# Performance work log

Measured on AMD Instinct MI355X. Metric: run time of the kernel, lower is better.

The kernel has to match this reference:

```python
import jax, jax.numpy as jnp
import numpy as np

B, T, F, H = 64, 512, 128, 512
NUM_LAYERS = 3


def _lstm_layer(x_tbf, W_ih, W_hh, b_ih, b_hh):
    # x_tbf: [T, B, in], W_ih: [4H, in], W_hh: [4H, H]
    # PyTorch gate order: i, f, g, o
    Hd = W_hh.shape[1]
    Bd = x_tbf.shape[1]
    # precompute input projections for all timesteps (one big GEMM)
    x_proj = jnp.einsum('tbf,gf->tbg', x_tbf, W_ih) + b_ih  # [T, B, 4H]

    def step(carry, xp_t):
        h, c = carry
        gates = xp_t + h @ W_hh.T + b_hh  # [B, 4H]
        i, f, g, o = jnp.split(gates, 4, axis=-1)
        i = jax.nn.sigmoid(i)
        f = jax.nn.sigmoid(f)
        g = jnp.tanh(g)
        o = jax.nn.sigmoid(o)
        c = f * c + i * g
        h = o * jnp.tanh(c)
        return (h, c), h

    h0 = jnp.zeros((Bd, Hd), x_tbf.dtype)
    c0 = jnp.zeros((Bd, Hd), x_tbf.dtype)
    _, hs = jax.lax.scan(step, (h0, c0), x_proj)
    return hs  # [T, B, H]


def setup_inputs() -> dict:
    key = jax.random.key(0)
    ks = jax.random.split(key, 20)
    s = 1.0 / np.sqrt(H)
    inp = {"input_tensor": jax.random.normal(ks[0], (B, T, F), jnp.float32)}
    in_dims = [F, H, H]
    ki = 1
    for l in range(NUM_LAYERS):
        inp[f"W_ih{l}"] = jax.random.uniform(ks[ki], (4 * H, in_dims[l]), jnp.float32, -s, s); ki += 1
        inp[f"W_hh{l}"] = jax.random.uniform(ks[ki], (4 * H, H), jnp.float32, -s, s); ki += 1
        inp[f"b_ih{l}"] = jax.random.uniform(ks[ki], (4 * H,), jnp.float32, -s, s); ki += 1
        inp[f"b_hh{l}"] = jax.random.uniform(ks[ki], (4 * H,), jnp.float32, -s, s); ki += 1
    s1 = 1.0 / np.sqrt(H)
    inp["fc_W1"] = jax.random.uniform(ks[13], (64, H), jnp.float32, -s1, s1)
    inp["fc_b1"] = jax.random.uniform(ks[14], (64,), jnp.float32, -s1, s1)
    s2 = 1.0 / np.sqrt(64)
    inp["fc_W2"] = jax.random.uniform(ks[15], (1, 64), jnp.float32, -s2, s2)
    inp["fc_b2"] = jax.random.uniform(ks[16], (1,), jnp.float32, -s2, s2)
    return inp


def reference(input_tensor, W_ih0, W_hh0, b_ih0, b_hh0,
              W_ih1, W_hh1, b_ih1, b_hh1,
              W_ih2, W_hh2, b_ih2, b_hh2,
              fc_W1, fc_b1, fc_W2, fc_b2):
    x = jnp.transpose(input_tensor, (1, 0, 2))  # [T, B, F]
    x = _lstm_layer(x, W_ih0, W_hh0, b_ih0, b_hh0)
    x = _lstm_layer(x, W_ih1, W_hh1, b_ih1, b_hh1)  # eval mode: no dropout
    x = _lstm_layer(x, W_ih2, W_hh2, b_ih2, b_hh2)
    last = x[-1]  # [B, H]
    h1 = jax.nn.relu(last @ fc_W1.T + fc_b1)
    out = jax.nn.relu(h1 @ fc_W2.T + fc_b2)  # [B, 1]
    return out
```

## Files before the change

### kernel.cpp

```cpp
#include <hip/hip_runtime.h>
#include <hip/hip_fp16.h>
#include <math.h>

#define B_ 64
#define T_ 512
#define F_ 128
#define H_ 512
#define NBLK 96
#define SPIN_MAX (1 << 23)

typedef _Float16 f16x8 __attribute__((ext_vector_type(8)));
typedef float f32x4 __attribute__((ext_vector_type(4)));
typedef int   i32x4 __attribute__((ext_vector_type(4)));

__device__ __forceinline__ unsigned short f2h(float f) {
    return __half_as_ushort(__float2half(f));
}
__device__ __forceinline__ float h2f(unsigned short u) {
    return __half2float(__ushort_as_half(u));
}

__global__ void transpose_x(const float* __restrict__ in, unsigned* __restrict__ xs) {
    const int t = blockIdx.x;
    for (int idx = threadIdx.x; idx < B_ * F_ / 4; idx += blockDim.x) {
        const int kp2 = idx >> 6;
        const int bb = idx & 63;
        const float* src = in + (size_t)bb * T_ * F_ + (size_t)t * F_ + 4 * kp2;
        const unsigned h0 = f2h(src[0]), h1 = f2h(src[1]);
        const unsigned h2 = f2h(src[2]), h3 = f2h(src[3]);
        const unsigned dw0 = h0 | (h1 << 16);
        const unsigned dw1 = h2 | (h3 << 16);
        *(unsigned long long*)(xs + (size_t)t * 4096 + (size_t)kp2 * 128 + bb * 2) =
            ((unsigned long long)dw1 << 32) | dw0;
    }
}

__device__ __forceinline__ float sigmoid_(float x) { return 1.0f / (1.0f + expf(-x)); }

__device__ __forceinline__ unsigned long long loadc_u64(const unsigned* p) {
    return __hip_atomic_load((const unsigned long long*)p, __ATOMIC_RELAXED,
                             __HIP_MEMORY_SCOPE_AGENT);
}
__device__ __forceinline__ unsigned loadc_u32(const unsigned* p) {
    return __hip_atomic_load(p, __ATOMIC_RELAXED, __HIP_MEMORY_SCOPE_AGENT);
}
__device__ __forceinline__ void storec_u64(unsigned* p, unsigned long long v) {
    __hip_atomic_store((unsigned long long*)p, v, __ATOMIC_RELAXED,
                       __HIP_MEMORY_SCOPE_AGENT);
}
__device__ __forceinline__ void storec_f(float* p, float v) {
    __hip_atomic_store(p, v, __ATOMIC_RELAXED, __HIP_MEMORY_SCOPE_AGENT);
}
__device__ __forceinline__ float loadc_f(const float* p) {
    return __hip_atomic_load(p, __ATOMIC_RELAXED, __HIP_MEMORY_SCOPE_AGENT);
}

__device__ __forceinline__ void gbar(int* __restrict__ slots, int* __restrict__ go,
                                     int bid, int tid, int e) {
    asm volatile("s_waitcnt vmcnt(0) lgkmcnt(0)" ::: "memory");
    __syncthreads();
    if (tid == 0)
        __hip_atomic_store(&slots[bid * 16], e, __ATOMIC_RELAXED,
                           __HIP_MEMORY_SCOPE_AGENT);
    if (bid == 0) {
        for (int s2 = tid; s2 < NBLK; s2 += 256) {
            int guard = 0;
            while (__hip_atomic_load(&slots[s2 * 16], __ATOMIC_RELAXED,
                                     __HIP_MEMORY_SCOPE_AGENT) < e &&
                   ++guard < SPIN_MAX)
                __builtin_amdgcn_s_sleep(1);
        }
        __syncthreads();
        if (tid == 0)
            __hip_atomic_store(go, e, __ATOMIC_RELAXED, __HIP_MEMORY_SCOPE_AGENT);
    } else if (tid == 0) {
        int guard = 0;
        while (__hip_atomic_load(go, __ATOMIC_RELAXED,
                                 __HIP_MEMORY_SCOPE_AGENT) < e &&
               ++guard < SPIN_MAX)
            __builtin_amdgcn_s_sleep(1);
    }
    __syncthreads();
}

template <int NKX, bool XCOH>
__device__ __forceinline__ void step_mfma(const unsigned* __restrict__ xs_l,
                                          const unsigned* __restrict__ hs_l,
                                          const unsigned short* wfrag,
                                          const int lane, f32x4 (&acc)[4]) {
    constexpr int NK = NKX + 16;
    unsigned long long v[8][2];

    auto load2 = [&](unsigned long long* d, int i) {
        const unsigned* p = (i < NKX) ? (xs_l + (size_t)i * 1024)
                                      : (hs_l + (size_t)(i - NKX) * 1024);
        if ((i < NKX) ? XCOH : true) {
            d[0] = loadc_u64(p);
            d[1] = loadc_u64(p + 128);
        } else {
            d[0] = *(const unsigned long long*)p;
            d[1] = *(const unsigned long long*)(p + 128);
        }
    };

#pragma unroll
    for (int p = 0; p < 8; ++p) load2(v[p], p);

#pragma unroll
    for (int i = 0; i < NK; ++i) {
        union Frag { i32x4 i4; f16x8 s; } Bf, A0, A1, A2, A3;
        const unsigned long long* d = v[i % 8];
        Bf.i4[0] = (int)(unsigned)d[0];
        Bf.i4[1] = (int)(unsigned)(d[0] >> 32);
        Bf.i4[2] = (int)(unsigned)d[1];
        Bf.i4[3] = (int)(unsigned)(d[1] >> 32);
        if (i + 8 < NK) load2(v[i % 8], i + 8);
        A0.i4 = *(const i32x4*)&wfrag[i * 2048 + lane * 8];
        A1.i4 = *(const i32x4*)&wfrag[i * 2048 + 512 + lane * 8];
        A2.i4 = *(const i32x4*)&wfrag[i * 2048 + 1024 + lane * 8];
        A3.i4 = *(const i32x4*)&wfrag[i * 2048 + 1536 + lane * 8];
        acc[0] = __builtin_amdgcn_mfma_f32_16x16x32_f16(A0.s, Bf.s, acc[0], 0, 0, 0);
        acc[1] = __builtin_amdgcn_mfma_f32_16x16x32_f16(A1.s, Bf.s, acc[1], 0, 0, 0);
        acc[2] = __builtin_amdgcn_mfma_f32_16x16x32_f16(A2.s, Bf.s, acc[2], 0, 0, 0);
        acc[3] = __builtin_amdgcn_mfma_f32_16x16x32_f16(A3.s, Bf.s, acc[3], 0, 0, 0);
    }
}

__global__ void __launch_bounds__(256, 1) lstm_scan(
    const unsigned* __restrict__ xs, unsigned* __restrict__ hb,
    float* __restrict__ h1s, float* __restrict__ out,
    int* __restrict__ bar_slots, int* __restrict__ bar_go,
    const float* __restrict__ Wih0, const float* __restrict__ Whh0,
    const float* __restrict__ bih0, const float* __restrict__ bhh0,
    const float* __restrict__ Wih1, const float* __restrict__ Whh1,
    const float* __restrict__ bih1, const float* __restrict__ bhh1,
    const float* __restrict__ Wih2, const float* __restrict__ Whh2,
    const float* __restrict__ bih2, const float* __restrict__ bhh2,
    const float* __restrict__ fcW1, const float* __restrict__ fcb1,
    const float* __restrict__ fcW2, const float* __restrict__ fcb2) {
    __shared__ unsigned short wfrag[32 * 2048];
    __shared__ float redsc[4 * 64];

    const float* WihA[3] = {Wih0, Wih1, Wih2};
    const float* WhhA[3] = {Whh0, Whh1, Whh2};
    const float* bihA[3] = {bih0, bih1, bih2};
    const float* bhhA[3] = {bhh0, bhh1, bhh2};

    const int tid   = threadIdx.x;
    const int bid   = blockIdx.x;
    const int layer = bid >> 5;
    const int cb    = bid & 31;
    const int c0    = cb * 16;
    const int lane  = tid & 63;
    const int w     = __builtin_amdgcn_readfirstlane(tid >> 6);
    const int KX    = (layer == 0) ? F_ : H_;
    const int NK    = KX / 32 + 16;

    const float* wih = WihA[layer];
    const float* whh = WhhA[layer];

    for (int idx = tid; idx < NK * 2048; idx += 256) {
        const int i = idx >> 11, rem = idx & 2047;
        const int rg = rem >> 9, r2 = rem & 511;
        const int l = r2 >> 3, j = r2 & 7;
        const int m = l & 15;
        const int grow = (m & 3) * 512 + c0 + rg * 4 + (m >> 2);
        const int k = i * 32 + (l >> 4) * 8 + j;
        const float f = (k < KX) ? wih[(size_t)grow * KX + k]
                                 : whh[(size_t)grow * 512 + (k - KX)];
        wfrag[i * 2048 + rg * 512 + l * 8 + j] = f2h(f);
    }
    __syncthreads();

    const int fb    = w * 16 + (lane & 15);
    const int q     = lane >> 4;
    float bias[4][4];
#pragma unroll
    for (int rg = 0; rg < 4; ++rg)
#pragma unroll
        for (int g = 0; g < 4; ++g)
            bias[rg][g] = bihA[layer][g * 512 + c0 + rg * 4 + q] +
                          bhhA[layer][g * 512 + c0 + rg * 4 + q];

    unsigned* hb_l = hb + (size_t)layer * 32768;
    const unsigned* hb_in = hb + (size_t)(layer - 1) * 32768;
    int hstore[4];
#pragma unroll
    for (int rg = 0; rg < 4; ++rg)
        hstore[rg] = (cb * 4 + rg) * 128 + fb * 2;

    float c_reg[4] = {0.0f, 0.0f, 0.0f, 0.0f};
    const int laneoff = q * 256 + fb * 2;

    for (int s = 0; s < T_ + 2; ++s) {
        const int t = s - layer;
        if (t >= 0 && t < T_) {
            const int p_out  = t & 1;
            const int p_prev = (t + 1) & 1;
            const unsigned* xs_l =
                ((layer == 0) ? (xs + (size_t)t * 4096)
                              : (hb_in + (size_t)p_out * 16384)) + laneoff;
            const unsigned* hs_l = hb_l + (size_t)p_prev * 16384 + laneoff;

            f32x4 acc[4] = {{0.f,0.f,0.f,0.f},{0.f,0.f,0.f,0.f},
                            {0.f,0.f,0.f,0.f},{0.f,0.f,0.f,0.f}};
            if (layer == 0) step_mfma<4, false>(xs_l, hs_l, wfrag, lane, acc);
            else            step_mfma<16, true>(xs_l, hs_l, wfrag, lane, acc);

#pragma unroll
            for (int rg = 0; rg < 4; ++rg) {
                float a[4];
#pragma unroll
                for (int g = 0; g < 4; ++g)
                    a[g] = bias[rg][g] + acc[rg][g];

                const float ig = sigmoid_(a[0]);
                const float fg = sigmoid_(a[1]);
                const float gg = tanhf(a[2]);
                const float og = sigmoid_(a[3]);
                c_reg[rg] = fg * c_reg[rg] + ig * gg;
                const float hv = og * tanhf(c_reg[rg]);

                const unsigned P0 = (unsigned)f2h(hv);
                const unsigned P1 = (unsigned)__shfl_xor((int)P0, 16, 64) & 0xFFFFu;
                const unsigned D  = P0 | (P1 << 16);
                const unsigned D2 = (unsigned)__shfl_xor((int)D, 32, 64);
                if (q == 0) {
                    storec_u64(&hb_l[(size_t)p_out * 16384 + hstore[rg]],
                               ((unsigned long long)D2 << 32) | D);
                }
            }
        }
        gbar(bar_slots, bar_go, bid, tid, s + 1);
    }

    const unsigned* h2u = hb + (size_t)2 * 32768 + 16384;
    const int fcb = tid & 63;
    if (bid < 64) {
        float part = 0.0f;
        const float* wrow = fcW1 + (size_t)bid * H_ + w * 128;
#pragma unroll 8
        for (int k = 0; k < 128; ++k) {
            const int kk = w * 128 + k;
            const unsigned dv =
                loadc_u32(h2u + (kk >> 2) * 128 + fcb * 2 + ((kk >> 1) & 1));
            const float val = h2f((unsigned short)((dv >> ((kk & 1) * 16)) & 0xFFFFu));
            part = fmaf(wrow[k], val, part);
        }
        redsc[w * 64 + fcb] = part;
        __syncthreads();
        if (tid < 64) {
            float acc2 = fcb1[bid] + redsc[tid] + redsc[64 + tid] +
                         redsc[128 + tid] + redsc[192 + tid];
            storec_f(&h1s[bid * B_ + tid], fmaxf(acc2, 0.0f));
        }
    }
    gbar(bar_slots, bar_go, bid, tid, T_ + 3);
    if (bid == 0 && tid < 64) {
        float acc2 = fcb2[0];
#pragma unroll
        for (int c = 0; c < 64; ++c)
            acc2 = fmaf(fcW2[c], loadc_f(&h1s[c * B_ + tid]), acc2);
        out[tid] = fmaxf(acc2, 0.0f);
    }
}

extern "C" void kernel_launch(void* const* d_in, const int* in_sizes, int n_in,
                              void* d_out, int out_size, void* d_ws, size_t ws_size,
                              hipStream_t stream) {
    const float* in    = (const float*)d_in[0];
    const float* Wih0  = (const float*)d_in[1];
    const float* Whh0  = (const float*)d_in[2];
    const float* bih0  = (const float*)d_in[3];
    const float* bhh0  = (const float*)d_in[4];
    const float* Wih1  = (const float*)d_in[5];
    const float* Whh1  = (const float*)d_in[6];
    const float* bih1  = (const float*)d_in[7];
    const float* bhh1  = (const float*)d_in[8];
    const float* Wih2  = (const float*)d_in[9];
    const float* Whh2  = (const float*)d_in[10];
    const float* bih2  = (const float*)d_in[11];
    const float* bhh2  = (const float*)d_in[12];
    const float* fcW1  = (const float*)d_in[13];
    const float* fcb1  = (const float*)d_in[14];
    const float* fcW2  = (const float*)d_in[15];
    const float* fcb2  = (const float*)d_in[16];
    float* outp = (float*)d_out;

    unsigned* xs  = (unsigned*)d_ws;
    unsigned* hbf = xs + (size_t)T_ * 4096;
    float*    h1s = (float*)(hbf + (size_t)3 * 32768);
    int*      bar = (int*)(h1s + 64 * 64);
    int*      bar_slots = bar;
    int*      bar_go    = bar + NBLK * 16;

    hipMemsetAsync(hbf, 0,
                   ((size_t)3 * 32768 + 64 * 64 + NBLK * 16 + 16) * sizeof(int),
                   stream);

    transpose_x<<<dim3(T_), dim3(256), 0, stream>>>(in, xs);

    void* args[] = {
        (void*)&xs, (void*)&hbf, (void*)&h1s, (void*)&outp,
        (void*)&bar_slots, (void*)&bar_go,
        (void*)&Wih0, (void*)&Whh0, (void*)&bih0, (void*)&bhh0,
        (void*)&Wih1, (void*)&Whh1, (void*)&bih1, (void*)&bhh1,
        (void*)&Wih2, (void*)&Whh2, (void*)&bih2, (void*)&bhh2,
        (void*)&fcW1, (void*)&fcb1, (void*)&fcW2, (void*)&fcb2};
    hipLaunchCooperativeKernel((void*)lstm_scan, dim3(NBLK), dim3(256), args, 0, stream);
}
```

Before: 3.228 ms.

## Use decentralized grid barrier, fast gate math, deeper operand prefetch

The grid barrier drops the centralized two-hop scheme, where block 0 polls every slot and then releases a go flag. Instead, every block polls all 96 slots directly, with one thread per slot, which removes a serialized round trip per timestep. Sigmoid and tanh now use fast exp plus the hardware reciprocal in place of libm expf and tanhf, cutting per-step latency in the gate epilogue. The B-fragment prefetch ring grows from 8 to 16 entries to hide more load latency, at the cost of more registers and extra barrier polling traffic on L2.

```diff
diff --git a/kernel.cpp b/kernel.cpp
--- a/kernel.cpp
+++ b/kernel.cpp
@@ -35,7 +35,12 @@
     }
 }
 
-__device__ __forceinline__ float sigmoid_(float x) { return 1.0f / (1.0f + expf(-x)); }
+__device__ __forceinline__ float sigmoid_(float x) {
+    return __builtin_amdgcn_rcpf(1.0f + __expf(-x));
+}
+__device__ __forceinline__ float tanh_(float x) {
+    return 1.0f - 2.0f * __builtin_amdgcn_rcpf(1.0f + __expf(2.0f * x));
+}
 
 __device__ __forceinline__ unsigned long long loadc_u64(const unsigned* p) {
     return __hip_atomic_load((const unsigned long long*)p, __ATOMIC_RELAXED,
@@ -55,27 +60,15 @@
     return __hip_atomic_load(p, __ATOMIC_RELAXED, __HIP_MEMORY_SCOPE_AGENT);
 }
 
-__device__ __forceinline__ void gbar(int* __restrict__ slots, int* __restrict__ go,
-                                     int bid, int tid, int e) {
+__device__ __forceinline__ void gbar(int* __restrict__ slots, int bid, int tid, int e) {
     asm volatile("s_waitcnt vmcnt(0) lgkmcnt(0)" ::: "memory");
     __syncthreads();
     if (tid == 0)
         __hip_atomic_store(&slots[bid * 16], e, __ATOMIC_RELAXED,
                            __HIP_MEMORY_SCOPE_AGENT);
-    if (bid == 0) {
-        for (int s2 = tid; s2 < NBLK; s2 += 256) {
-            int guard = 0;
-            while (__hip_atomic_load(&slots[s2 * 16], __ATOMIC_RELAXED,
-                                     __HIP_MEMORY_SCOPE_AGENT) < e &&
-                   ++guard < SPIN_MAX)
-                __builtin_amdgcn_s_sleep(1);
-        }
-        __syncthreads();
-        if (tid == 0)
-            __hip_atomic_store(go, e, __ATOMIC_RELAXED, __HIP_MEMORY_SCOPE_AGENT);
-    } else if (tid == 0) {
+    if (tid < NBLK) {
         int guard = 0;
-        while (__hip_atomic_load(go, __ATOMIC_RELAXED,
+        while (__hip_atomic_load(&slots[tid * 16], __ATOMIC_RELAXED,
                                  __HIP_MEMORY_SCOPE_AGENT) < e &&
                ++guard < SPIN_MAX)
             __builtin_amdgcn_s_sleep(1);
@@ -89,7 +82,8 @@
                                           const unsigned short* wfrag,
                                           const int lane, f32x4 (&acc)[4]) {
     constexpr int NK = NKX + 16;
-    unsigned long long v[8][2];
+    constexpr int PD = 16;
+    unsigned long long v[PD][2];
 
     auto load2 = [&](unsigned long long* d, int i) {
         const unsigned* p = (i < NKX) ? (xs_l + (size_t)i * 1024)
@@ -104,17 +98,17 @@
     };
 
 #pragma unroll
-    for (int p = 0; p < 8; ++p) load2(v[p], p);
+    for (int p = 0; p < PD; ++p) load2(v[p], p);
 
 #pragma unroll
     for (int i = 0; i < NK; ++i) {
         union Frag { i32x4 i4; f16x8 s; } Bf, A0, A1, A2, A3;
-        const unsigned long long* d = v[i % 8];
+        const unsigned long long* d = v[i % PD];
         Bf.i4[0] = (int)(unsigned)d[0];
         Bf.i4[1] = (int)(unsigned)(d[0] >> 32);
         Bf.i4[2] = (int)(unsigned)d[1];
         Bf.i4[3] = (int)(unsigned)(d[1] >> 32);
-        if (i + 8 < NK) load2(v[i % 8], i + 8);
+        if (i + PD < NK) load2(v[i % PD], i + PD);
         A0.i4 = *(const i32x4*)&wfrag[i * 2048 + lane * 8];
         A1.i4 = *(const i32x4*)&wfrag[i * 2048 + 512 + lane * 8];
         A2.i4 = *(const i32x4*)&wfrag[i * 2048 + 1024 + lane * 8];
@@ -216,10 +210,10 @@
 
                 const float ig = sigmoid_(a[0]);
                 const float fg = sigmoid_(a[1]);
-                const float gg = tanhf(a[2]);
+                const float gg = tanh_(a[2]);
                 const float og = sigmoid_(a[3]);
                 c_reg[rg] = fg * c_reg[rg] + ig * gg;
-                const float hv = og * tanhf(c_reg[rg]);
+                const float hv = og * tanh_(c_reg[rg]);
 
                 const unsigned P0 = (unsigned)f2h(hv);
                 const unsigned P1 = (unsigned)__shfl_xor((int)P0, 16, 64) & 0xFFFFu;
@@ -231,7 +225,7 @@
                 }
             }
         }
-        gbar(bar_slots, bar_go, bid, tid, s + 1);
+        gbar(bar_slots, bid, tid, s + 1);
     }
 
     const unsigned* h2u = hb + (size_t)2 * 32768 + 16384;
@@ -255,7 +249,7 @@
             storec_f(&h1s[bid * B_ + tid], fmaxf(acc2, 0.0f));
         }
     }
-    gbar(bar_slots, bar_go, bid, tid, T_ + 3);
+    gbar(bar_slots, bid, tid, T_ + 3);
     if (bid == 0 && tid < 64) {
         float acc2 = fcb2[0];
 #pragma unroll
```

After: 2.620 ms. -18.8%, faster.
